# Optimization experiments

Measured on AMD Instinct MI355X. Metric: run time of the kernel, lower is better.

Reference implementation:

```python
import jax, jax.numpy as jnp
import numpy as np

VOCAB = 23
PAD_IDX = 21
SOS_IDX = 22
LATENT = 128
COND = 16
HID = 1024
EMB = 512
MAX_LEN = 64
B = 4096


def setup_inputs() -> dict:
    key = jax.random.key(0)
    ks = jax.random.split(key, 12)
    s = lambda *d: 1.0 / np.sqrt(d[-1])
    inp = {
        "z": jax.random.normal(ks[0], (B, LATENT), jnp.float32),
        "cond": jax.random.normal(ks[1], (B, COND), jnp.float32),
        "emb_table": jax.random.normal(ks[2], (VOCAB, EMB), jnp.float32),
        "W_lh": jax.random.uniform(ks[3], (HID, LATENT + COND), jnp.float32, -s(LATENT + COND), s(LATENT + COND)),
        "b_lh": jax.random.uniform(ks[4], (HID,), jnp.float32, -s(LATENT + COND), s(LATENT + COND)),
        "W_ih": jax.random.uniform(ks[5], (4 * HID, EMB), jnp.float32, -s(HID), s(HID)),
        "W_hh": jax.random.uniform(ks[6], (4 * HID, HID), jnp.float32, -s(HID), s(HID)),
        "b_ih": jax.random.uniform(ks[7], (4 * HID,), jnp.float32, -s(HID), s(HID)),
        "b_hh": jax.random.uniform(ks[8], (4 * HID,), jnp.float32, -s(HID), s(HID)),
        "W_out": jax.random.uniform(ks[9], (VOCAB, HID), jnp.float32, -s(HID), s(HID)),
        "b_out": jax.random.uniform(ks[10], (VOCAB,), jnp.float32, -s(HID), s(HID)),
    }
    return inp


def reference(z, cond, emb_table, W_lh, b_lh, W_ih, W_hh, b_ih, b_hh, W_out, b_out):
    # padding_idx row of the embedding is zero (and non-trainable in torch)
    E = emb_table.at[PAD_IDX].set(0.0)
    # initial hidden from latent+cond; initial cell is zeros
    h0 = jnp.concatenate([z, cond], axis=1) @ W_lh.T + b_lh          # [B, H]
    c0 = jnp.zeros_like(h0)
    x0 = E[jnp.full((z.shape[0],), SOS_IDX, dtype=jnp.int32)]        # [B, E]
    bias = b_ih + b_hh

    def step(carry, _):
        h, c, x = carry
        gates = x @ W_ih.T + h @ W_hh.T + bias                        # [B, 4H]
        i, f, g, o = jnp.split(gates, 4, axis=1)
        i = jax.nn.sigmoid(i)
        f = jax.nn.sigmoid(f)
        g = jnp.tanh(g)
        o = jax.nn.sigmoid(o)
        c = f * c + i * g
        h = o * jnp.tanh(c)
        logits = h @ W_out.T + b_out                                  # [B, V]
        nxt = jnp.argmax(logits, axis=1)                              # greedy token
        x = E[nxt]
        return (h, c, x), logits

    _, logits_t = jax.lax.scan(step, (h0, c0, x0), None, length=MAX_LEN)  # [T, B, V]
    return jnp.transpose(logits_t, (1, 0, 2))                         # [B, T, V]
```

## Files before the change

kernel.cpp:

```cpp
#include <hip/hip_runtime.h>

#define NB 4096
#define NH 1024
#define NE 512
#define NV 23
#define NT 64
#define NL 144
#define PADV 21
#define SOSV 22

typedef unsigned short u16;
typedef __attribute__((ext_vector_type(16))) float f32x16;
typedef __attribute__((ext_vector_type(8))) __bf16 bf16x8;
typedef __attribute__((ext_vector_type(8))) unsigned short u16x8;

__device__ __forceinline__ u16 f2bf(float x) {
  unsigned u = __float_as_uint(x);
  u += 0x7FFFu + ((u >> 16) & 1u);
  return (u16)(u >> 16);
}
__device__ __forceinline__ float bf2f(u16 h) {
  return __uint_as_float(((unsigned)h) << 16);
}

__device__ __forceinline__ size_t hidx(int m, int j) {
  return ((size_t)(((m >> 8) * 32 + (j >> 5)) * 4 + ((j >> 3) & 3)) * 2048)
         + (size_t)((m & 255) * 8) + (j & 7);
}

__global__ void prep_kernel(const float* __restrict__ Whh, u16* __restrict__ Whi,
                            u16* __restrict__ Wlo, float* __restrict__ c,
                            int* __restrict__ tok) {
  int i = blockIdx.x * 256 + threadIdx.x;
  float wv = Whh[i];
  u16 hi = f2bf(wv);
  u16 lo = f2bf(wv - bf2f(hi));
  const int nw = i >> 10, k = i & 1023;
  const int g = nw >> 10, jcol = nw & 1023;
  const int jt = jcol >> 6, jl = jcol & 63;
  const int row = g * 64 + jl;
  const size_t oi = ((size_t)((jt * 32 + (k >> 5)) * 4 + ((k >> 3) & 3)) * 2048)
                    + (size_t)(row * 8) + (k & 7);
  Whi[oi] = hi;
  Wlo[oi] = lo;
  c[i] = 0.0f;
  if (i < NB) tok[i] = SOSV;
}

__global__ void exw_kernel(const float* __restrict__ emb, const float* __restrict__ Wih,
                           const float* __restrict__ bih, const float* __restrict__ bhh,
                           float* __restrict__ ExW) {
  __shared__ float Es[NE];
  const int v = blockIdx.y;
  const int n = blockIdx.x * 256 + threadIdx.x;
  for (int k = threadIdx.x; k < NE; k += 256)
    Es[k] = (v == PADV) ? 0.0f : emb[v * NE + k];
  __syncthreads();
  float s = bih[n] + bhh[n];
  const float* wr = Wih + (long)n * NE;
  for (int k = 0; k < NE; ++k) s = fmaf(Es[k], wr[k], s);
  ExW[v * (4 * NH) + n] = s;
}

__global__ void h0_kernel(const float* __restrict__ z, const float* __restrict__ cnd,
                          const float* __restrict__ Wlh, const float* __restrict__ blh,
                          u16* __restrict__ hhi, u16* __restrict__ hlo) {
  __shared__ float zc[8][NL];
  const int b0 = blockIdx.y * 8;
  const int j = blockIdx.x * 256 + threadIdx.x;
  for (int idx = threadIdx.x; idx < 8 * NL; idx += 256) {
    int bi = idx / NL, k = idx % NL;
    zc[bi][k] = (k < 128) ? z[(long)(b0 + bi) * 128 + k]
                          : cnd[(long)(b0 + bi) * 16 + (k - 128)];
  }
  __syncthreads();
  float acc[8];
  const float bj = blh[j];
#pragma unroll
  for (int bi = 0; bi < 8; ++bi) acc[bi] = bj;
  const float* wr = Wlh + (long)j * NL;
  for (int k = 0; k < NL; ++k) {
    float wv = wr[k];
#pragma unroll
    for (int bi = 0; bi < 8; ++bi) acc[bi] = fmaf(wv, zc[bi][k], acc[bi]);
  }
#pragma unroll
  for (int bi = 0; bi < 8; ++bi) {
    size_t idx = hidx(b0 + bi, j);
    u16 hi = f2bf(acc[bi]);
    hhi[idx] = hi;
    hlo[idx] = f2bf(acc[bi] - bf2f(hi));
  }
}

__device__ __forceinline__ void stage8(const u16* __restrict__ src, u16* dst) {
#pragma unroll
  for (int i = 0; i < 8; ++i)
    __builtin_amdgcn_global_load_lds(
        (const __attribute__((address_space(1))) void*)(src + i * 512),
        (__attribute__((address_space(3))) void*)(dst + i * 512), 16, 0, 0);
}

__global__ __launch_bounds__(512, 2)
void gates_cell_kernel(const u16* __restrict__ Whi, const u16* __restrict__ Wlo,
                       const u16* __restrict__ hhi_in, const u16* __restrict__ hlo_in,
                       const float* __restrict__ ExW, const int* __restrict__ tok,
                       float* __restrict__ c, u16* __restrict__ hhi_out,
                       u16* __restrict__ hlo_out) {
  __shared__ u16 lds[65536];

  const int bid = blockIdx.x;
  const int swz = (bid & 7) * 32 + (bid >> 3);
  const int jt = swz >> 4;
  const int mt = swz & 15;
  const int m0 = mt << 8;
  const int j0 = jt << 6;

  const int tid = threadIdx.x;
  const int w = tid >> 6, l = tid & 63;
  const int wm = w >> 1, wn = w & 1;
  const int col = l & 31, h5 = l >> 5;

  const int mat = w >> 1, hf = w & 1;
  const u16* simg = (mat == 0) ? hhi_in : (mat == 1) ? hlo_in : (mat == 2) ? Whi : Wlo;
  const size_t sbase = ((mat < 2) ? ((size_t)mt * 262144) : ((size_t)jt * 262144))
                       + (size_t)hf * 4096 + (size_t)l * 8;
  const u16* sit = simg + sbase;
  u16* dwave = (u16*)lds + mat * 16384 + hf * 4096;

  f32x16 acc[2][4];
#pragma unroll
  for (int mi = 0; mi < 2; ++mi)
#pragma unroll
    for (int g = 0; g < 4; ++g)
#pragma unroll
      for (int r = 0; r < 16; ++r) acc[mi][g][r] = 0.f;

  stage8(sit, dwave);
  __syncthreads();

  for (int ks = 0; ks < 32; ++ks) {
    const int buf = ks & 1;
    if (ks < 31) stage8(sit + (size_t)(ks + 1) * 8192, dwave + (buf ^ 1) * 8192);

    const u16* abase = lds + buf * 8192;
    const u16* bbase = lds + 32768 + buf * 8192;

#pragma unroll
    for (int kk = 0; kk < 2; ++kk) {
      const int ko = (kk * 2 + h5) * 2048;
      bf16x8 ah[2], al[2], bh[4], bl[4];
#pragma unroll
      for (int mi = 0; mi < 2; ++mi) {
        const int ao = ko + (wm * 64 + mi * 32 + col) * 8;
        ah[mi] = *reinterpret_cast<const bf16x8*>(abase + ao);
        al[mi] = *reinterpret_cast<const bf16x8*>(abase + 16384 + ao);
      }
#pragma unroll
      for (int g = 0; g < 4; ++g) {
        const int bo = ko + (g * 64 + wn * 32 + col) * 8;
        bh[g] = *reinterpret_cast<const bf16x8*>(bbase + bo);
        bl[g] = *reinterpret_cast<const bf16x8*>(bbase + 16384 + bo);
      }
#pragma unroll
      for (int g = 0; g < 4; ++g)
#pragma unroll
        for (int mi = 0; mi < 2; ++mi)
          acc[mi][g] = __builtin_amdgcn_mfma_f32_32x32x16_bf16(ah[mi], bh[g], acc[mi][g], 0, 0, 0);
#pragma unroll
      for (int g = 0; g < 4; ++g)
#pragma unroll
        for (int mi = 0; mi < 2; ++mi)
          acc[mi][g] = __builtin_amdgcn_mfma_f32_32x32x16_bf16(ah[mi], bl[g], acc[mi][g], 0, 0, 0);
#pragma unroll
      for (int g = 0; g < 4; ++g)
#pragma unroll
        for (int mi = 0; mi < 2; ++mi)
          acc[mi][g] = __builtin_amdgcn_mfma_f32_32x32x16_bf16(al[mi], bh[g], acc[mi][g], 0, 0, 0);
    }
    __syncthreads();
  }

  const int j = j0 + wn * 32 + col;
#pragma unroll
  for (int mi = 0; mi < 2; ++mi) {
#pragma unroll
    for (int r = 0; r < 16; ++r) {
      const int row = (r & 3) + ((r >> 2) << 3) + (h5 << 2);
      const int m = m0 + wm * 64 + mi * 32 + row;
      const int tk = tok[m];
      const float* exr = ExW + (size_t)tk * 4096;
      const float gi = acc[mi][0][r] + exr[j];
      const float gf = acc[mi][1][r] + exr[NH + j];
      const float gg = acc[mi][2][r] + exr[2 * NH + j];
      const float go = acc[mi][3][r] + exr[3 * NH + j];
      const float i_ = 1.0f / (1.0f + expf(-gi));
      const float f_ = 1.0f / (1.0f + expf(-gf));
      const float g_ = tanhf(gg);
      const float o_ = 1.0f / (1.0f + expf(-go));
      const size_t cidx = (size_t)m * NH + j;
      const float cn = f_ * c[cidx] + i_ * g_;
      c[cidx] = cn;
      const float hn = o_ * tanhf(cn);
      const u16 hi = f2bf(hn);
      const size_t oidx = hidx(m, j);
      hhi_out[oidx] = hi;
      hlo_out[oidx] = f2bf(hn - bf2f(hi));
    }
  }
}

__global__ __launch_bounds__(256)
void logits_kernel(const u16* __restrict__ hhi, const u16* __restrict__ hlo,
                   const float* __restrict__ Wout, const float* __restrict__ bout,
                   float* __restrict__ out, int* __restrict__ tok, int t) {
  __shared__ float hs[8][NH];
  __shared__ float part[8][24][8];
  __shared__ float lg[8][24];
  const int b0 = blockIdx.x * 8;
  const int tid = threadIdx.x;
  for (int ci = tid; ci < 1024; ci += 256) {
    const int bi = ci >> 7, cj = ci & 127;
    const int m = b0 + bi;
    const int ks = cj >> 2, qq = cj & 3;
    const size_t base = ((size_t)(((m >> 8) * 32 + ks) * 4 + qq) * 2048)
                        + (size_t)((m & 255) * 8);
    const u16x8 vh = *reinterpret_cast<const u16x8*>(hhi + base);
    const u16x8 vl = *reinterpret_cast<const u16x8*>(hlo + base);
    const int kb = ks * 32 + qq * 8;
#pragma unroll
    for (int e = 0; e < 8; ++e) hs[bi][kb + e] = bf2f(vh[e]) + bf2f(vl[e]);
  }
  __syncthreads();
  const int v = tid & 31, kc = tid >> 5;
  if (v < NV) {
    float s[8];
#pragma unroll
    for (int bi = 0; bi < 8; ++bi) s[bi] = 0.f;
    const float* wr = Wout + (long)v * NH + kc * 128;
    const int kb = kc * 128;
    for (int k = 0; k < 128; ++k) {
      float wv = wr[k];
#pragma unroll
      for (int bi = 0; bi < 8; ++bi) s[bi] = fmaf(wv, hs[bi][kb + k], s[bi]);
    }
#pragma unroll
    for (int bi = 0; bi < 8; ++bi) part[kc][v][bi] = s[bi];
  }
  __syncthreads();
  if (tid < NV * 8) {
    const int vv = tid >> 3, bi = tid & 7;
    float s = bout[vv];
#pragma unroll
    for (int k = 0; k < 8; ++k) s += part[k][vv][bi];
    lg[bi][vv] = s;
    out[((long)(b0 + bi) * NT + t) * NV + vv] = s;
  }
  __syncthreads();
  if (tid < 8) {
    float best = lg[tid][0];
    int bv = 0;
    for (int vv = 1; vv < NV; ++vv) {
      float x = lg[tid][vv];
      if (x > best) { best = x; bv = vv; }
    }
    tok[b0 + tid] = bv;
  }
}

extern "C" void kernel_launch(void* const* d_in, const int* in_sizes, int n_in,
                              void* d_out, int out_size, void* d_ws, size_t ws_size,
                              hipStream_t stream) {
  const float* z    = (const float*)d_in[0];
  const float* cnd  = (const float*)d_in[1];
  const float* emb  = (const float*)d_in[2];
  const float* Wlh  = (const float*)d_in[3];
  const float* blh  = (const float*)d_in[4];
  const float* Wih  = (const float*)d_in[5];
  const float* Whh  = (const float*)d_in[6];
  const float* bih  = (const float*)d_in[7];
  const float* bhh  = (const float*)d_in[8];
  const float* Wout = (const float*)d_in[9];
  const float* bout = (const float*)d_in[10];
  float* out = (float*)d_out;

  char* ws = (char*)d_ws;
  size_t off = 0;
  auto alloc = [&](size_t bytes) -> void* {
    off = (off + 255) & ~(size_t)255;
    void* p = ws + off;
    off += bytes;
    return p;
  };
  u16* Whi = (u16*)alloc((size_t)4 * NH * NH * 2);
  u16* Wlo = (u16*)alloc((size_t)4 * NH * NH * 2);
  float* ExW = (float*)alloc((size_t)NV * 4 * NH * 4);
  u16* hhi0 = (u16*)alloc((size_t)NB * NH * 2);
  u16* hhi1 = (u16*)alloc((size_t)NB * NH * 2);
  u16* hlo0 = (u16*)alloc((size_t)NB * NH * 2);
  u16* hlo1 = (u16*)alloc((size_t)NB * NH * 2);
  float* cbuf = (float*)alloc((size_t)NB * NH * 4);
  int* tokb = (int*)alloc((size_t)NB * 4);
  u16* hhi[2] = {hhi0, hhi1};
  u16* hlo[2] = {hlo0, hlo1};

  prep_kernel<<<dim3((4 * NH * NH) / 256), dim3(256), 0, stream>>>(Whh, Whi, Wlo, cbuf, tokb);
  exw_kernel<<<dim3((4 * NH) / 256, NV), dim3(256), 0, stream>>>(emb, Wih, bih, bhh, ExW);
  h0_kernel<<<dim3(NH / 256, NB / 8), dim3(256), 0, stream>>>(z, cnd, Wlh, blh, hhi[0], hlo[0]);

  int p = 0;
  for (int t = 0; t < NT; ++t) {
    gates_cell_kernel<<<dim3(256), dim3(512), 0, stream>>>(
        Whi, Wlo, hhi[p], hlo[p], ExW, tokb, cbuf, hhi[p ^ 1], hlo[p ^ 1]);
    logits_kernel<<<dim3(NB / 8), dim3(256), 0, stream>>>(
        hhi[p ^ 1], hlo[p ^ 1], Wout, bout, out, tokb, t);
    p ^= 1;
  }
}
```

Before: 7.154 ms.

## Switch gates GEMM to 16x16x32 MFMA with 4 waves and larger per-wave tiles

Restructures the recurrent gate GEMM to use 256-thread blocks with 4 waves, each computing a 128x64 tile through 8x8 grids of 16x16x32 bf16 MFMAs. Previously 8 waves each held a 64x32 tile using 32x32x16 MFMAs. Each wave now stages one whole operand matrix into LDS with 16 async loads per step. The larger per-wave tile raises register reuse of the LDS fragments and cuts LDS reads per MFMA. The cost is heavy register pressure from 256 accumulator floats plus 32 fragment vectors, which may force occupancy to one block per CU or cause spills, and fewer waves are left to hide latency.

Result: slower. 9.813 ms (+37.2%).

```diff
diff --git a/kernel.cpp b/kernel.cpp
--- a/kernel.cpp
+++ b/kernel.cpp
@@ -10,7 +10,7 @@
 #define SOSV 22
 
 typedef unsigned short u16;
-typedef __attribute__((ext_vector_type(16))) float f32x16;
+typedef __attribute__((ext_vector_type(4))) float f32x4;
 typedef __attribute__((ext_vector_type(8))) __bf16 bf16x8;
 typedef __attribute__((ext_vector_type(8))) unsigned short u16x8;
 
@@ -93,15 +93,7 @@
   }
 }
 
-__device__ __forceinline__ void stage8(const u16* __restrict__ src, u16* dst) {
-#pragma unroll
-  for (int i = 0; i < 8; ++i)
-    __builtin_amdgcn_global_load_lds(
-        (const __attribute__((address_space(1))) void*)(src + i * 512),
-        (__attribute__((address_space(3))) void*)(dst + i * 512), 16, 0, 0);
-}
-
-__global__ __launch_bounds__(512, 2)
+__global__ __launch_bounds__(256, 1)
 void gates_cell_kernel(const u16* __restrict__ Whi, const u16* __restrict__ Wlo,
                        const u16* __restrict__ hhi_in, const u16* __restrict__ hlo_in,
                        const float* __restrict__ ExW, const int* __restrict__ tok,
@@ -119,93 +111,100 @@
   const int tid = threadIdx.x;
   const int w = tid >> 6, l = tid & 63;
   const int wm = w >> 1, wn = w & 1;
-  const int col = l & 31, h5 = l >> 5;
-
-  const int mat = w >> 1, hf = w & 1;
-  const u16* simg = (mat == 0) ? hhi_in : (mat == 1) ? hlo_in : (mat == 2) ? Whi : Wlo;
-  const size_t sbase = ((mat < 2) ? ((size_t)mt * 262144) : ((size_t)jt * 262144))
-                       + (size_t)hf * 4096 + (size_t)l * 8;
+  const int q = l >> 4, rL = l & 15;
+
+  const u16* simg = (w == 0) ? hhi_in : (w == 1) ? hlo_in : (w == 2) ? Whi : Wlo;
+  const size_t sbase = ((w < 2) ? ((size_t)mt * 262144) : ((size_t)jt * 262144))
+                       + (size_t)l * 8;
   const u16* sit = simg + sbase;
-  u16* dwave = (u16*)lds + mat * 16384 + hf * 4096;
-
-  f32x16 acc[2][4];
-#pragma unroll
-  for (int mi = 0; mi < 2; ++mi)
-#pragma unroll
-    for (int g = 0; g < 4; ++g)
-#pragma unroll
-      for (int r = 0; r < 16; ++r) acc[mi][g][r] = 0.f;
-
-  stage8(sit, dwave);
+  u16* dwave = (u16*)lds + w * 16384 + l * 8;
+
+  f32x4 acc[8][8];
+#pragma unroll
+  for (int mi = 0; mi < 8; ++mi)
+#pragma unroll
+    for (int n = 0; n < 8; ++n) acc[mi][n] = (f32x4){0.f, 0.f, 0.f, 0.f};
+
+#pragma unroll
+  for (int i = 0; i < 16; ++i)
+    __builtin_amdgcn_global_load_lds(
+        (const __attribute__((address_space(1))) void*)(sit + i * 512),
+        (__attribute__((address_space(3))) void*)(dwave + i * 512), 16, 0, 0);
   __syncthreads();
 
   for (int ks = 0; ks < 32; ++ks) {
     const int buf = ks & 1;
-    if (ks < 31) stage8(sit + (size_t)(ks + 1) * 8192, dwave + (buf ^ 1) * 8192);
-
-    const u16* abase = lds + buf * 8192;
-    const u16* bbase = lds + 32768 + buf * 8192;
-
-#pragma unroll
-    for (int kk = 0; kk < 2; ++kk) {
-      const int ko = (kk * 2 + h5) * 2048;
-      bf16x8 ah[2], al[2], bh[4], bl[4];
-#pragma unroll
-      for (int mi = 0; mi < 2; ++mi) {
-        const int ao = ko + (wm * 64 + mi * 32 + col) * 8;
-        ah[mi] = *reinterpret_cast<const bf16x8*>(abase + ao);
-        al[mi] = *reinterpret_cast<const bf16x8*>(abase + 16384 + ao);
-      }
-#pragma unroll
-      for (int g = 0; g < 4; ++g) {
-        const int bo = ko + (g * 64 + wn * 32 + col) * 8;
-        bh[g] = *reinterpret_cast<const bf16x8*>(bbase + bo);
-        bl[g] = *reinterpret_cast<const bf16x8*>(bbase + 16384 + bo);
-      }
-#pragma unroll
-      for (int g = 0; g < 4; ++g)
-#pragma unroll
-        for (int mi = 0; mi < 2; ++mi)
-          acc[mi][g] = __builtin_amdgcn_mfma_f32_32x32x16_bf16(ah[mi], bh[g], acc[mi][g], 0, 0, 0);
-#pragma unroll
-      for (int g = 0; g < 4; ++g)
-#pragma unroll
-        for (int mi = 0; mi < 2; ++mi)
-          acc[mi][g] = __builtin_amdgcn_mfma_f32_32x32x16_bf16(ah[mi], bl[g], acc[mi][g], 0, 0, 0);
-#pragma unroll
-      for (int g = 0; g < 4; ++g)
-#pragma unroll
-        for (int mi = 0; mi < 2; ++mi)
-          acc[mi][g] = __builtin_amdgcn_mfma_f32_32x32x16_bf16(al[mi], bh[g], acc[mi][g], 0, 0, 0);
-    }
+    if (ks < 31) {
+      const u16* src = sit + (size_t)(ks + 1) * 8192;
+      u16* dst = dwave + (buf ^ 1) * 8192;
+#pragma unroll
+      for (int i = 0; i < 16; ++i)
+        __builtin_amdgcn_global_load_lds(
+            (const __attribute__((address_space(1))) void*)(src + i * 512),
+            (__attribute__((address_space(3))) void*)(dst + i * 512), 16, 0, 0);
+    }
+
+    const int qoff = buf * 8192 + q * 2048;
+    bf16x8 ah[8], al[8], bh[8], bl[8];
+#pragma unroll
+    for (int mi = 0; mi < 8; ++mi) {
+      const int ao = qoff + (wm * 128 + mi * 16 + rL) * 8;
+      ah[mi] = *reinterpret_cast<const bf16x8*>(lds + ao);
+      al[mi] = *reinterpret_cast<const bf16x8*>(lds + 16384 + ao);
+    }
+#pragma unroll
+    for (int n = 0; n < 8; ++n) {
+      const int row = (n >> 1) * 64 + wn * 32 + (n & 1) * 16 + rL;
+      const int bo = qoff + row * 8;
+      bh[n] = *reinterpret_cast<const bf16x8*>(lds + 32768 + bo);
+      bl[n] = *reinterpret_cast<const bf16x8*>(lds + 49152 + bo);
+    }
+#pragma unroll
+    for (int n = 0; n < 8; ++n)
+#pragma unroll
+      for (int mi = 0; mi < 8; ++mi)
+        acc[mi][n] = __builtin_amdgcn_mfma_f32_16x16x32_bf16(ah[mi], bh[n], acc[mi][n], 0, 0, 0);
+#pragma unroll
+    for (int n = 0; n < 8; ++n)
+#pragma unroll
+      for (int mi = 0; mi < 8; ++mi)
+        acc[mi][n] = __builtin_amdgcn_mfma_f32_16x16x32_bf16(ah[mi], bl[n], acc[mi][n], 0, 0, 0);
+#pragma unroll
+    for (int n = 0; n < 8; ++n)
+#pragma unroll
+      for (int mi = 0; mi < 8; ++mi)
+        acc[mi][n] = __builtin_amdgcn_mfma_f32_16x16x32_bf16(al[mi], bh[n], acc[mi][n], 0, 0, 0);
+
     __syncthreads();
   }
 
-  const int j = j0 + wn * 32 + col;
-#pragma unroll
-  for (int mi = 0; mi < 2; ++mi) {
-#pragma unroll
-    for (int r = 0; r < 16; ++r) {
-      const int row = (r & 3) + ((r >> 2) << 3) + (h5 << 2);
-      const int m = m0 + wm * 64 + mi * 32 + row;
+#pragma unroll
+  for (int mi = 0; mi < 8; ++mi) {
+#pragma unroll
+    for (int r = 0; r < 4; ++r) {
+      const int m = m0 + wm * 128 + mi * 16 + q * 4 + r;
       const int tk = tok[m];
       const float* exr = ExW + (size_t)tk * 4096;
-      const float gi = acc[mi][0][r] + exr[j];
-      const float gf = acc[mi][1][r] + exr[NH + j];
-      const float gg = acc[mi][2][r] + exr[2 * NH + j];
-      const float go = acc[mi][3][r] + exr[3 * NH + j];
-      const float i_ = 1.0f / (1.0f + expf(-gi));
-      const float f_ = 1.0f / (1.0f + expf(-gf));
-      const float g_ = tanhf(gg);
-      const float o_ = 1.0f / (1.0f + expf(-go));
-      const size_t cidx = (size_t)m * NH + j;
-      const float cn = f_ * c[cidx] + i_ * g_;
-      c[cidx] = cn;
-      const float hn = o_ * tanhf(cn);
-      const u16 hi = f2bf(hn);
-      const size_t oidx = hidx(m, j);
-      hhi_out[oidx] = hi;
-      hlo_out[oidx] = f2bf(hn - bf2f(hi));
+#pragma unroll
+      for (int jh = 0; jh < 2; ++jh) {
+        const int j = j0 + wn * 32 + jh * 16 + rL;
+        const float gi = acc[mi][0 * 2 + jh][r] + exr[j];
+        const float gf = acc[mi][1 * 2 + jh][r] + exr[NH + j];
+        const float gg = acc[mi][2 * 2 + jh][r] + exr[2 * NH + j];
+        const float go = acc[mi][3 * 2 + jh][r] + exr[3 * NH + j];
+        const float i_ = 1.0f / (1.0f + expf(-gi));
+        const float f_ = 1.0f / (1.0f + expf(-gf));
+        const float g_ = tanhf(gg);
+        const float o_ = 1.0f / (1.0f + expf(-go));
+        const size_t cidx = (size_t)m * NH + j;
+        const float cn = f_ * c[cidx] + i_ * g_;
+        c[cidx] = cn;
+        const float hn = o_ * tanhf(cn);
+        const u16 hi = f2bf(hn);
+        const size_t oidx = hidx(m, j);
+        hhi_out[oidx] = hi;
+        hlo_out[oidx] = f2bf(hn - bf2f(hi));
+      }
     }
   }
 }
@@ -310,7 +309,7 @@
 
   int p = 0;
   for (int t = 0; t < NT; ++t) {
-    gates_cell_kernel<<<dim3(256), dim3(512), 0, stream>>>(
+    gates_cell_kernel<<<dim3(256), dim3(256), 0, stream>>>(
         Whi, Wlo, hhi[p], hlo[p], ExW, tokb, cbuf, hhi[p ^ 1], hlo[p ^ 1]);
     logits_kernel<<<dim3(NB / 8), dim3(256), 0, stream>>>(
         hhi[p ^ 1], hlo[p ^ 1], Wout, bout, out, tokb, t);
```
